# Kernel optimization log

Measured on AMD Instinct MI355X. Metric: run time of the kernel, lower is better.

## Reference

```python
import jax, jax.numpy as jnp
import numpy as np

N = 131072   # octree nodes at this depth
K = 27       # 3x3x3 kernel taps
CIN = 32
COUT = 32
EPS = 1e-5   # BatchNorm1d default eps


def setup_inputs() -> dict:
    key = jax.random.key(0)
    k1, k2, k3, k4, k5 = jax.random.split(key, 5)
    data = jax.random.normal(k1, (N, CIN), dtype=jnp.float32)
    # deconv weight: one [Cin, Cout] matrix per kernel tap
    weight = jax.random.normal(k2, (K, CIN, COUT), dtype=jnp.float32) * 0.05
    gamma = 1.0 + 0.1 * jax.random.normal(k3, (COUT,), dtype=jnp.float32)
    beta = 0.1 * jax.random.normal(k4, (COUT,), dtype=jnp.float32)
    # octree neighbor table: for each input node, the K output nodes it scatters into
    neigh = jax.random.randint(k5, (N, K), 0, N, dtype=jnp.int32)
    return {"data": data, "weight": weight, "gamma": gamma, "beta": beta, "neigh": neigh}


def reference(data, weight, gamma, beta, neigh):
    # Sparse transposed conv (stride=1): each node i produces a contribution
    # data[i] @ weight[k] that is scatter-added into output node neigh[i, k].
    contrib = jnp.einsum('ni,kio->nko', data, weight)          # [N, K, Cout]
    out = jax.ops.segment_sum(contrib.reshape(-1, COUT),
                              neigh.reshape(-1),
                              num_segments=N)                   # [N, Cout]
    # BatchNorm1d (training mode: batch statistics over the node dimension)
    mean = jnp.mean(out, axis=0)
    var = jnp.var(out, axis=0)
    y = gamma * (out - mean) * jax.lax.rsqrt(var + EPS) + beta
    # ReLU
    return jnp.maximum(y, 0.0)
```

## Files before the change

kernel.cpp:

```cpp
#include <hip/hip_runtime.h>
#include <hip/hip_bf16.h>
#include <hip/hip_fp16.h>

#define NN 131072
#define KK 27
#define CC 32
#define EPSV 1e-5f

#define WS_STATS 0
#define WS_ACC   256
#define WS_NEEDED ((size_t)WS_ACC + (size_t)NN * CC * 2)

typedef __bf16 bf16x8 __attribute__((ext_vector_type(8)));
typedef short s16x8 __attribute__((ext_vector_type(8)));
typedef float f32x4 __attribute__((ext_vector_type(4)));

__device__ inline unsigned short f2bf(float f) {
    unsigned int u = __float_as_uint(f);
    u += 0x7FFF + ((u >> 16) & 1);
    return (unsigned short)(u >> 16);
}

__global__ __launch_bounds__(256) void scatter_kernel(
    const float* __restrict__ data, const float* __restrict__ weight,
    const int* __restrict__ neigh, __half2* __restrict__ acc2)
{
    __shared__ unsigned short wfrag[KK * 2 * 64 * 8];

    const int tid = threadIdx.x;
    const int lane = tid & 63;
    const int wv = tid >> 6;
    const int node_base = blockIdx.x * 128;

    for (int p = tid; p < KK * 1024; p += 256) {
        const int k  = p >> 10;
        const int ci = (p >> 5) & 31;
        const int c  = p & 31;
        const unsigned short v = f2bf(weight[p]);
        const int chalf = c & 1;
        const int col   = c >> 1;
        const int fl = col | ((ci >> 3) << 4);
        const int j = ci & 7;
        wfrag[(((k << 1) | chalf) * 64 + fl) * 8 + j] = v;
    }

    const int quad = lane >> 4;
    const int m = lane & 15;
    s16x8 afr[2];
    #pragma unroll
    for (int g = 0; g < 2; ++g) {
        const int node = node_base + wv * 32 + g * 16 + m;
        const float* src = data + node * 32 + quad * 8;
        const float4 v0 = *(const float4*)(src);
        const float4 v1 = *(const float4*)(src + 4);
        s16x8 s;
        s[0] = (short)f2bf(v0.x); s[1] = (short)f2bf(v0.y);
        s[2] = (short)f2bf(v0.z); s[3] = (short)f2bf(v0.w);
        s[4] = (short)f2bf(v1.x); s[5] = (short)f2bf(v1.y);
        s[6] = (short)f2bf(v1.z); s[7] = (short)f2bf(v1.w);
        afr[g] = s;
    }

    __syncthreads();

    const int rq = quad << 2;
    const f32x4 zero = {0.f, 0.f, 0.f, 0.f};

    for (int k = 0; k < KK; ++k) {
        int nj[2][4];
        #pragma unroll
        for (int g = 0; g < 2; ++g)
            #pragma unroll
            for (int r = 0; r < 4; ++r) {
                const int node = node_base + wv * 32 + g * 16 + rq + r;
                nj[g][r] = neigh[node * KK + k];
            }
        const s16x8 bs0 = *(const s16x8*)&wfrag[(((k << 1) | 0) * 64 + lane) * 8];
        const s16x8 bs1 = *(const s16x8*)&wfrag[(((k << 1) | 1) * 64 + lane) * 8];
        #pragma unroll
        for (int g = 0; g < 2; ++g) {
            const f32x4 d0 = __builtin_amdgcn_mfma_f32_16x16x32_bf16(
                __builtin_bit_cast(bf16x8, afr[g]), __builtin_bit_cast(bf16x8, bs0),
                zero, 0, 0, 0);
            const f32x4 d1 = __builtin_amdgcn_mfma_f32_16x16x32_bf16(
                __builtin_bit_cast(bf16x8, afr[g]), __builtin_bit_cast(bf16x8, bs1),
                zero, 0, 0, 0);
            #pragma unroll
            for (int r = 0; r < 4; ++r) {
                __half2 v;
                v.x = __float2half(d0[r]);
                v.y = __float2half(d1[r]);
                unsafeAtomicAdd(&acc2[nj[g][r] * 16 + m], v);
            }
        }
    }
}

__global__ __launch_bounds__(256) void stats_kernel(
    const __half2* __restrict__ acc2, float* __restrict__ stats)
{
    __shared__ float ls[16][33], ls2[16][33];
    const int tid = threadIdx.x;
    const int c2 = tid & 15, rg = tid >> 4;
    float sx = 0.f, sy = 0.f, s2x = 0.f, s2y = 0.f;
    const int row0 = blockIdx.x * 512;
    for (int it = 0; it < 32; ++it) {
        const __half2 h = acc2[(row0 + it * 16 + rg) * 16 + c2];
        const float vx = __half2float(h.x), vy = __half2float(h.y);
        sx += vx; sy += vy; s2x += vx * vx; s2y += vy * vy;
    }
    ls[rg][2 * c2] = sx;  ls[rg][2 * c2 + 1] = sy;
    ls2[rg][2 * c2] = s2x; ls2[rg][2 * c2 + 1] = s2y;
    __syncthreads();
    if (tid < 32) {
        float S = 0.f, S2 = 0.f;
        #pragma unroll
        for (int g = 0; g < 16; ++g) { S += ls[g][tid]; S2 += ls2[g][tid]; }
        atomicAdd(&stats[tid], S);
        atomicAdd(&stats[32 + tid], S2);
    }
}

__global__ __launch_bounds__(256) void bn_relu_kernel(
    const __half2* __restrict__ acc2, float* __restrict__ out,
    const float* __restrict__ stats,
    const float* __restrict__ gamma, const float* __restrict__ beta)
{
    __shared__ float sc[32], sh[32];
    const int tid = threadIdx.x;
    if (tid < 32) {
        const float mean = stats[tid] * (1.0f / NN);
        const float var  = stats[32 + tid] * (1.0f / NN) - mean * mean;
        const float s = gamma[tid] * rsqrtf(var + EPSV);
        sc[tid] = s;
        sh[tid] = beta[tid] - mean * s;
    }
    __syncthreads();
    const int idx = blockIdx.x * 256 + tid;
    const int c0 = (idx & 3) << 3;
    const __half2 h4[4] = { acc2[idx * 4], acc2[idx * 4 + 1],
                            acc2[idx * 4 + 2], acc2[idx * 4 + 3] };
    float4 o0, o1;
    o0.x = fmaxf(__half2float(h4[0].x) * sc[c0]     + sh[c0],     0.f);
    o0.y = fmaxf(__half2float(h4[0].y) * sc[c0 + 1] + sh[c0 + 1], 0.f);
    o0.z = fmaxf(__half2float(h4[1].x) * sc[c0 + 2] + sh[c0 + 2], 0.f);
    o0.w = fmaxf(__half2float(h4[1].y) * sc[c0 + 3] + sh[c0 + 3], 0.f);
    o1.x = fmaxf(__half2float(h4[2].x) * sc[c0 + 4] + sh[c0 + 4], 0.f);
    o1.y = fmaxf(__half2float(h4[2].y) * sc[c0 + 5] + sh[c0 + 5], 0.f);
    o1.z = fmaxf(__half2float(h4[3].x) * sc[c0 + 6] + sh[c0 + 6], 0.f);
    o1.w = fmaxf(__half2float(h4[3].y) * sc[c0 + 7] + sh[c0 + 7], 0.f);
    ((float4*)out)[idx * 2]     = o0;
    ((float4*)out)[idx * 2 + 1] = o1;
}

__global__ __launch_bounds__(256) void scatter_f32_kernel(
    const float* __restrict__ data, const float* __restrict__ weight,
    const int* __restrict__ neigh, float* __restrict__ out)
{
    __shared__ unsigned short wfrag[KK * 2 * 64 * 8];
    const int tid = threadIdx.x;
    const int lane = tid & 63;
    const int wv = tid >> 6;
    const int node_base = blockIdx.x * 128;
    for (int p = tid; p < KK * 1024; p += 256) {
        const int k  = p >> 10;
        const int ci = (p >> 5) & 31;
        const int c  = p & 31;
        const unsigned short v = f2bf(weight[p]);
        const int chalf = c >> 4;
        const int fl = (c & 15) | ((ci >> 3) << 4);
        const int j = ci & 7;
        wfrag[(((k << 1) | chalf) * 64 + fl) * 8 + j] = v;
    }
    const int quad = lane >> 4;
    const int m = lane & 15;
    s16x8 afr[2];
    #pragma unroll
    for (int g = 0; g < 2; ++g) {
        const int node = node_base + wv * 32 + g * 16 + m;
        const float* src = data + node * 32 + quad * 8;
        const float4 v0 = *(const float4*)(src);
        const float4 v1 = *(const float4*)(src + 4);
        s16x8 s;
        s[0] = (short)f2bf(v0.x); s[1] = (short)f2bf(v0.y);
        s[2] = (short)f2bf(v0.z); s[3] = (short)f2bf(v0.w);
        s[4] = (short)f2bf(v1.x); s[5] = (short)f2bf(v1.y);
        s[6] = (short)f2bf(v1.z); s[7] = (short)f2bf(v1.w);
        afr[g] = s;
    }
    __syncthreads();
    const int rq = quad << 2;
    const f32x4 zero = {0.f, 0.f, 0.f, 0.f};
    for (int k = 0; k < KK; ++k) {
        int nj[2][4];
        #pragma unroll
        for (int g = 0; g < 2; ++g)
            #pragma unroll
            for (int r = 0; r < 4; ++r) {
                const int node = node_base + wv * 32 + g * 16 + rq + r;
                nj[g][r] = neigh[node * KK + k];
            }
        #pragma unroll
        for (int ch = 0; ch < 2; ++ch) {
            const s16x8 bs = *(const s16x8*)&wfrag[((((k << 1) | ch)) * 64 + lane) * 8];
            const bf16x8 bfr = __builtin_bit_cast(bf16x8, bs);
            const int c = (ch << 4) | m;
            #pragma unroll
            for (int g = 0; g < 2; ++g) {
                f32x4 a2 = __builtin_amdgcn_mfma_f32_16x16x32_bf16(
                    __builtin_bit_cast(bf16x8, afr[g]), bfr, zero, 0, 0, 0);
                #pragma unroll
                for (int r = 0; r < 4; ++r)
                    __hip_atomic_fetch_add(&out[nj[g][r] * 32 + c], a2[r],
                                           __ATOMIC_RELAXED, __HIP_MEMORY_SCOPE_AGENT);
            }
        }
    }
}

__global__ __launch_bounds__(256) void stats_f32_kernel(
    const float* __restrict__ out, float* __restrict__ stats)
{
    __shared__ float ls[256], ls2[256];
    const int tid = threadIdx.x;
    const int c = tid & 31, rg = tid >> 5;
    float s = 0.f, s2 = 0.f;
    const int row0 = blockIdx.x * 512;
    for (int it = 0; it < 64; ++it) {
        const float v = out[(row0 + it * 8 + rg) * 32 + c];
        s += v; s2 += v * v;
    }
    ls[tid] = s; ls2[tid] = s2;
    __syncthreads();
    if (tid < 32) {
        float S = 0.f, S2 = 0.f;
        #pragma unroll
        for (int r = 0; r < 8; ++r) { S += ls[r * 32 + tid]; S2 += ls2[r * 32 + tid]; }
        atomicAdd(&stats[tid], S);
        atomicAdd(&stats[32 + tid], S2);
    }
}

__global__ __launch_bounds__(256) void bn_relu_f32_kernel(
    float* __restrict__ out, const float* __restrict__ stats,
    const float* __restrict__ gamma, const float* __restrict__ beta)
{
    __shared__ float sc[32], sh[32];
    const int tid = threadIdx.x;
    if (tid < 32) {
        const float mean = stats[tid] * (1.0f / NN);
        const float var  = stats[32 + tid] * (1.0f / NN) - mean * mean;
        const float s = gamma[tid] * rsqrtf(var + EPSV);
        sc[tid] = s;
        sh[tid] = beta[tid] - mean * s;
    }
    __syncthreads();
    const int idx = blockIdx.x * 256 + tid;
    float4 v = ((float4*)out)[idx];
    const int cb = (idx & 7) << 2;
    v.x = fmaxf(v.x * sc[cb]     + sh[cb],     0.f);
    v.y = fmaxf(v.y * sc[cb + 1] + sh[cb + 1], 0.f);
    v.z = fmaxf(v.z * sc[cb + 2] + sh[cb + 2], 0.f);
    v.w = fmaxf(v.w * sc[cb + 3] + sh[cb + 3], 0.f);
    ((float4*)out)[idx] = v;
}

extern "C" void kernel_launch(void* const* d_in, const int* in_sizes, int n_in,
                              void* d_out, int out_size, void* d_ws, size_t ws_size,
                              hipStream_t stream) {
    const float* data   = (const float*)d_in[0];
    const float* weight = (const float*)d_in[1];
    const float* gamma  = (const float*)d_in[2];
    const float* beta   = (const float*)d_in[3];
    const int*   neigh  = (const int*)d_in[4];
    float* out = (float*)d_out;
    char* ws = (char*)d_ws;
    float* stats = (float*)(ws + WS_STATS);

    if (ws_size >= WS_NEEDED) {
        __half2* acc2 = (__half2*)(ws + WS_ACC);
        hipMemsetAsync(ws, 0, WS_NEEDED, stream);
        scatter_kernel<<<NN / 128, 256, 0, stream>>>(data, weight, neigh, acc2);
        stats_kernel<<<NN / 512, 256, 0, stream>>>(acc2, stats);
        bn_relu_kernel<<<(NN * CC / 8) / 256, 256, 0, stream>>>(acc2, out, stats, gamma, beta);
    } else {
        hipMemsetAsync(out, 0, (size_t)NN * CC * sizeof(float), stream);
        hipMemsetAsync(stats, 0, 64 * sizeof(float), stream);
        scatter_f32_kernel<<<NN / 128, 256, 0, stream>>>(data, weight, neigh, out);
        stats_f32_kernel<<<NN / 512, 256, 0, stream>>>(out, stats);
        bn_relu_f32_kernel<<<(NN * CC / 4) / 256, 256, 0, stream>>>(out, stats, gamma, beta);
    }
}
```

Measured before the change: 271.6 us.

## Precompute bf16 weight fragments once and software-pipeline neighbor/weight loads

Adds a small prep kernel that converts and permutes the weights into MFMA fragment layout in workspace once, so each of the 1024 scatter blocks no longer rebuilds a 55KB LDS copy and waits on a barrier. The scatter kernel now reads weight fragments straight from global/L2 and prefetches the next tap's neighbor indices and weight fragments while the current tap's MFMAs and atomics run. This removes the per-block prologue and frees LDS for occupancy, at the cost of an extra launch, two memsets instead of one, and L2 traffic for the weight reads.

```diff
diff --git a/kernel.cpp b/kernel.cpp
--- a/kernel.cpp
+++ b/kernel.cpp
@@ -8,7 +8,8 @@
 #define EPSV 1e-5f
 
 #define WS_STATS 0
-#define WS_ACC   256
+#define WS_WPERM 256
+#define WS_ACC   65536
 #define WS_NEEDED ((size_t)WS_ACC + (size_t)NN * CC * 2)
 
 typedef __bf16 bf16x8 __attribute__((ext_vector_type(8)));
@@ -21,29 +22,186 @@
     return (unsigned short)(u >> 16);
 }
 
+__global__ __launch_bounds__(256) void prep_weights_kernel(
+    const float* __restrict__ weight, unsigned short* __restrict__ wperm)
+{
+    const int p = blockIdx.x * 256 + threadIdx.x;
+    if (p >= KK * 1024) return;
+    const int k  = p >> 10;
+    const int ci = (p >> 5) & 31;
+    const int c  = p & 31;
+    const unsigned short v = f2bf(weight[p]);
+    const int chalf = c & 1;
+    const int col   = c >> 1;
+    const int fl = col | ((ci >> 3) << 4);
+    const int j = ci & 7;
+    wperm[(((k << 1) | chalf) * 64 + fl) * 8 + j] = v;
+}
+
 __global__ __launch_bounds__(256) void scatter_kernel(
+    const float* __restrict__ data, const unsigned short* __restrict__ wperm,
+    const int* __restrict__ neigh, __half2* __restrict__ acc2)
+{
+    const int tid = threadIdx.x;
+    const int lane = tid & 63;
+    const int wv = tid >> 6;
+    const int node_base = blockIdx.x * 128 + wv * 32;
+
+    const int quad = lane >> 4;
+    const int m = lane & 15;
+    const int rq = quad << 2;
+
+    s16x8 afr[2];
+    #pragma unroll
+    for (int g = 0; g < 2; ++g) {
+        const int node = node_base + g * 16 + m;
+        const float* src = data + node * 32 + quad * 8;
+        const float4 v0 = *(const float4*)(src);
+        const float4 v1 = *(const float4*)(src + 4);
+        s16x8 s;
+        s[0] = (short)f2bf(v0.x); s[1] = (short)f2bf(v0.y);
+        s[2] = (short)f2bf(v0.z); s[3] = (short)f2bf(v0.w);
+        s[4] = (short)f2bf(v1.x); s[5] = (short)f2bf(v1.y);
+        s[6] = (short)f2bf(v1.z); s[7] = (short)f2bf(v1.w);
+        afr[g] = s;
+    }
+
+    const s16x8* wp = (const s16x8*)wperm;
+    const f32x4 zero = {0.f, 0.f, 0.f, 0.f};
+
+    int nj0[4], nj1[4];
+    #pragma unroll
+    for (int r = 0; r < 4; ++r) {
+        nj0[r] = neigh[(node_base + rq + r) * KK];
+        nj1[r] = neigh[(node_base + 16 + rq + r) * KK];
+    }
+    s16x8 bs0 = wp[lane];
+    s16x8 bs1 = wp[64 + lane];
+
+    for (int k = 0; k < KK; ++k) {
+        const int kn = (k < KK - 1) ? k + 1 : k;
+        int nn0[4], nn1[4];
+        #pragma unroll
+        for (int r = 0; r < 4; ++r) {
+            nn0[r] = neigh[(node_base + rq + r) * KK + kn];
+            nn1[r] = neigh[(node_base + 16 + rq + r) * KK + kn];
+        }
+        const s16x8 nbs0 = wp[(kn * 2) * 64 + lane];
+        const s16x8 nbs1 = wp[(kn * 2 + 1) * 64 + lane];
+
+        {
+            const f32x4 d0 = __builtin_amdgcn_mfma_f32_16x16x32_bf16(
+                __builtin_bit_cast(bf16x8, afr[0]), __builtin_bit_cast(bf16x8, bs0),
+                zero, 0, 0, 0);
+            const f32x4 d1 = __builtin_amdgcn_mfma_f32_16x16x32_bf16(
+                __builtin_bit_cast(bf16x8, afr[0]), __builtin_bit_cast(bf16x8, bs1),
+                zero, 0, 0, 0);
+            #pragma unroll
+            for (int r = 0; r < 4; ++r) {
+                __half2 v;
+                v.x = __float2half(d0[r]);
+                v.y = __float2half(d1[r]);
+                unsafeAtomicAdd(&acc2[nj0[r] * 16 + m], v);
+            }
+        }
+        {
+            const f32x4 d0 = __builtin_amdgcn_mfma_f32_16x16x32_bf16(
+                __builtin_bit_cast(bf16x8, afr[1]), __builtin_bit_cast(bf16x8, bs0),
+                zero, 0, 0, 0);
+            const f32x4 d1 = __builtin_amdgcn_mfma_f32_16x16x32_bf16(
+                __builtin_bit_cast(bf16x8, afr[1]), __builtin_bit_cast(bf16x8, bs1),
+                zero, 0, 0, 0);
+            #pragma unroll
+            for (int r = 0; r < 4; ++r) {
+                __half2 v;
+                v.x = __float2half(d0[r]);
+                v.y = __float2half(d1[r]);
+                unsafeAtomicAdd(&acc2[nj1[r] * 16 + m], v);
+            }
+        }
+
+        bs0 = nbs0; bs1 = nbs1;
+        #pragma unroll
+        for (int r = 0; r < 4; ++r) { nj0[r] = nn0[r]; nj1[r] = nn1[r]; }
+    }
+}
+
+__global__ __launch_bounds__(256) void stats_kernel(
+    const __half2* __restrict__ acc2, float* __restrict__ stats)
+{
+    __shared__ float ls[16][33], ls2[16][33];
+    const int tid = threadIdx.x;
+    const int c2 = tid & 15, rg = tid >> 4;
+    float sx = 0.f, sy = 0.f, s2x = 0.f, s2y = 0.f;
+    const int row0 = blockIdx.x * 512;
+    for (int it = 0; it < 32; ++it) {
+        const __half2 h = acc2[(row0 + it * 16 + rg) * 16 + c2];
+        const float vx = __half2float(h.x), vy = __half2float(h.y);
+        sx += vx; sy += vy; s2x += vx * vx; s2y += vy * vy;
+    }
+    ls[rg][2 * c2] = sx;  ls[rg][2 * c2 + 1] = sy;
+    ls2[rg][2 * c2] = s2x; ls2[rg][2 * c2 + 1] = s2y;
+    __syncthreads();
+    if (tid < 32) {
+        float S = 0.f, S2 = 0.f;
+        #pragma unroll
+        for (int g = 0; g < 16; ++g) { S += ls[g][tid]; S2 += ls2[g][tid]; }
+        atomicAdd(&stats[tid], S);
+        atomicAdd(&stats[32 + tid], S2);
+    }
+}
+
+__global__ __launch_bounds__(256) void bn_relu_kernel(
+    const __half2* __restrict__ acc2, float* __restrict__ out,
+    const float* __restrict__ stats,
+    const float* __restrict__ gamma, const float* __restrict__ beta)
+{
+    __shared__ float sc[32], sh[32];
+    const int tid = threadIdx.x;
+    if (tid < 32) {
+        const float mean = stats[tid] * (1.0f / NN);
+        const float var  = stats[32 + tid] * (1.0f / NN) - mean * mean;
+        const float s = gamma[tid] * rsqrtf(var + EPSV);
+        sc[tid] = s;
+        sh[tid] = beta[tid] - mean * s;
+    }
+    __syncthreads();
+    const int idx = blockIdx.x * 256 + tid;
+    const int c0 = (idx & 3) << 3;
+    const __half2 h4[4] = { acc2[idx * 4], acc2[idx * 4 + 1],
+                            acc2[idx * 4 + 2], acc2[idx * 4 + 3] };
+    float4 o0, o1;
+    o0.x = fmaxf(__half2float(h4[0].x) * sc[c0]     + sh[c0],     0.f);
+    o0.y = fmaxf(__half2float(h4[0].y) * sc[c0 + 1] + sh[c0 + 1], 0.f);
+    o0.z = fmaxf(__half2float(h4[1].x) * sc[c0 + 2] + sh[c0 + 2], 0.f);
+    o0.w = fmaxf(__half2float(h4[1].y) * sc[c0 + 3] + sh[c0 + 3], 0.f);
+    o1.x = fmaxf(__half2float(h4[2].x) * sc[c0 + 4] + sh[c0 + 4], 0.f);
+    o1.y = fmaxf(__half2float(h4[2].y) * sc[c0 + 5] + sh[c0 + 5], 0.f);
+    o1.z = fmaxf(__half2float(h4[3].x) * sc[c0 + 6] + sh[c0 + 6], 0.f);
+    o1.w = fmaxf(__half2float(h4[3].y) * sc[c0 + 7] + sh[c0 + 7], 0.f);
+    ((float4*)out)[idx * 2]     = o0;
+    ((float4*)out)[idx * 2 + 1] = o1;
+}
+
+__global__ __launch_bounds__(256) void scatter_f32_kernel(
     const float* __restrict__ data, const float* __restrict__ weight,
-    const int* __restrict__ neigh, __half2* __restrict__ acc2)
+    const int* __restrict__ neigh, float* __restrict__ out)
 {
     __shared__ unsigned short wfrag[KK * 2 * 64 * 8];
-
     const int tid = threadIdx.x;
     const int lane = tid & 63;
     const int wv = tid >> 6;
     const int node_base = blockIdx.x * 128;
-
     for (int p = tid; p < KK * 1024; p += 256) {
         const int k  = p >> 10;
         const int ci = (p >> 5) & 31;
         const int c  = p & 31;
         const unsigned short v = f2bf(weight[p]);
-        const int chalf = c & 1;
-        const int col   = c >> 1;
-        const int fl = col | ((ci >> 3) << 4);
+        const int chalf = c >> 4;
+        const int fl = (c & 15) | ((ci >> 3) << 4);
         const int j = ci & 7;
         wfrag[(((k << 1) | chalf) * 64 + fl) * 8 + j] = v;
     }
-
     const int quad = lane >> 4;
     const int m = lane & 15;
     s16x8 afr[2];
@@ -60,134 +218,6 @@
         s[6] = (short)f2bf(v1.z); s[7] = (short)f2bf(v1.w);
         afr[g] = s;
     }
-
-    __syncthreads();
-
-    const int rq = quad << 2;
-    const f32x4 zero = {0.f, 0.f, 0.f, 0.f};
-
-    for (int k = 0; k < KK; ++k) {
-        int nj[2][4];
-        #pragma unroll
-        for (int g = 0; g < 2; ++g)
-            #pragma unroll
-            for (int r = 0; r < 4; ++r) {
-                const int node = node_base + wv * 32 + g * 16 + rq + r;
-                nj[g][r] = neigh[node * KK + k];
-            }
-        const s16x8 bs0 = *(const s16x8*)&wfrag[(((k << 1) | 0) * 64 + lane) * 8];
-        const s16x8 bs1 = *(const s16x8*)&wfrag[(((k << 1) | 1) * 64 + lane) * 8];
-        #pragma unroll
-        for (int g = 0; g < 2; ++g) {
-            const f32x4 d0 = __builtin_amdgcn_mfma_f32_16x16x32_bf16(
-                __builtin_bit_cast(bf16x8, afr[g]), __builtin_bit_cast(bf16x8, bs0),
-                zero, 0, 0, 0);
-            const f32x4 d1 = __builtin_amdgcn_mfma_f32_16x16x32_bf16(
-                __builtin_bit_cast(bf16x8, afr[g]), __builtin_bit_cast(bf16x8, bs1),
-                zero, 0, 0, 0);
-            #pragma unroll
-            for (int r = 0; r < 4; ++r) {
-                __half2 v;
-                v.x = __float2half(d0[r]);
-                v.y = __float2half(d1[r]);
-                unsafeAtomicAdd(&acc2[nj[g][r] * 16 + m], v);
-            }
-        }
-    }
-}
-
-__global__ __launch_bounds__(256) void stats_kernel(
-    const __half2* __restrict__ acc2, float* __restrict__ stats)
-{
-    __shared__ float ls[16][33], ls2[16][33];
-    const int tid = threadIdx.x;
-    const int c2 = tid & 15, rg = tid >> 4;
-    float sx = 0.f, sy = 0.f, s2x = 0.f, s2y = 0.f;
-    const int row0 = blockIdx.x * 512;
-    for (int it = 0; it < 32; ++it) {
-        const __half2 h = acc2[(row0 + it * 16 + rg) * 16 + c2];
-        const float vx = __half2float(h.x), vy = __half2float(h.y);
-        sx += vx; sy += vy; s2x += vx * vx; s2y += vy * vy;
-    }
-    ls[rg][2 * c2] = sx;  ls[rg][2 * c2 + 1] = sy;
-    ls2[rg][2 * c2] = s2x; ls2[rg][2 * c2 + 1] = s2y;
-    __syncthreads();
-    if (tid < 32) {
-        float S = 0.f, S2 = 0.f;
-        #pragma unroll
-        for (int g = 0; g < 16; ++g) { S += ls[g][tid]; S2 += ls2[g][tid]; }
-        atomicAdd(&stats[tid], S);
-        atomicAdd(&stats[32 + tid], S2);
-    }
-}
-
-__global__ __launch_bounds__(256) void bn_relu_kernel(
-    const __half2* __restrict__ acc2, float* __restrict__ out,
-    const float* __restrict__ stats,
-    const float* __restrict__ gamma, const float* __restrict__ beta)
-{
-    __shared__ float sc[32], sh[32];
-    const int tid = threadIdx.x;
-    if (tid < 32) {
-        const float mean = stats[tid] * (1.0f / NN);
-        const float var  = stats[32 + tid] * (1.0f / NN) - mean * mean;
-        const float s = gamma[tid] * rsqrtf(var + EPSV);
-        sc[tid] = s;
-        sh[tid] = beta[tid] - mean * s;
-    }
-    __syncthreads();
-    const int idx = blockIdx.x * 256 + tid;
-    const int c0 = (idx & 3) << 3;
-    const __half2 h4[4] = { acc2[idx * 4], acc2[idx * 4 + 1],
-                            acc2[idx * 4 + 2], acc2[idx * 4 + 3] };
-    float4 o0, o1;
-    o0.x = fmaxf(__half2float(h4[0].x) * sc[c0]     + sh[c0],     0.f);
-    o0.y = fmaxf(__half2float(h4[0].y) * sc[c0 + 1] + sh[c0 + 1], 0.f);
-    o0.z = fmaxf(__half2float(h4[1].x) * sc[c0 + 2] + sh[c0 + 2], 0.f);
-    o0.w = fmaxf(__half2float(h4[1].y) * sc[c0 + 3] + sh[c0 + 3], 0.f);
-    o1.x = fmaxf(__half2float(h4[2].x) * sc[c0 + 4] + sh[c0 + 4], 0.f);
-    o1.y = fmaxf(__half2float(h4[2].y) * sc[c0 + 5] + sh[c0 + 5], 0.f);
-    o1.z = fmaxf(__half2float(h4[3].x) * sc[c0 + 6] + sh[c0 + 6], 0.f);
-    o1.w = fmaxf(__half2float(h4[3].y) * sc[c0 + 7] + sh[c0 + 7], 0.f);
-    ((float4*)out)[idx * 2]     = o0;
-    ((float4*)out)[idx * 2 + 1] = o1;
-}
-
-__global__ __launch_bounds__(256) void scatter_f32_kernel(
-    const float* __restrict__ data, const float* __restrict__ weight,
-    const int* __restrict__ neigh, float* __restrict__ out)
-{
-    __shared__ unsigned short wfrag[KK * 2 * 64 * 8];
-    const int tid = threadIdx.x;
-    const int lane = tid & 63;
-    const int wv = tid >> 6;
-    const int node_base = blockIdx.x * 128;
-    for (int p = tid; p < KK * 1024; p += 256) {
-        const int k  = p >> 10;
-        const int ci = (p >> 5) & 31;
-        const int c  = p & 31;
-        const unsigned short v = f2bf(weight[p]);
-        const int chalf = c >> 4;
-        const int fl = (c & 15) | ((ci >> 3) << 4);
-        const int j = ci & 7;
-        wfrag[(((k << 1) | chalf) * 64 + fl) * 8 + j] = v;
-    }
-    const int quad = lane >> 4;
-    const int m = lane & 15;
-    s16x8 afr[2];
-    #pragma unroll
-    for (int g = 0; g < 2; ++g) {
-        const int node = node_base + wv * 32 + g * 16 + m;
-        const float* src = data + node * 32 + quad * 8;
-        const float4 v0 = *(const float4*)(src);
-        const float4 v1 = *(const float4*)(src + 4);
-        s16x8 s;
-        s[0] = (short)f2bf(v0.x); s[1] = (short)f2bf(v0.y);
-        s[2] = (short)f2bf(v0.z); s[3] = (short)f2bf(v0.w);
-        s[4] = (short)f2bf(v1.x); s[5] = (short)f2bf(v1.y);
-        s[6] = (short)f2bf(v1.z); s[7] = (short)f2bf(v1.w);
-        afr[g] = s;
-    }
     __syncthreads();
     const int rq = quad << 2;
     const f32x4 zero = {0.f, 0.f, 0.f, 0.f};
@@ -279,8 +309,11 @@
 
     if (ws_size >= WS_NEEDED) {
         __half2* acc2 = (__half2*)(ws + WS_ACC);
-        hipMemsetAsync(ws, 0, WS_NEEDED, stream);
-        scatter_kernel<<<NN / 128, 256, 0, stream>>>(data, weight, neigh, acc2);
+        unsigned short* wperm = (unsigned short*)(ws + WS_WPERM);
+        hipMemsetAsync(ws + WS_STATS, 0, 256, stream);
+        hipMemsetAsync(ws + WS_ACC, 0, (size_t)NN * CC * 2, stream);
+        prep_weights_kernel<<<(KK * 1024 + 255) / 256, 256, 0, stream>>>(weight, wperm);
+        scatter_kernel<<<NN / 128, 256, 0, stream>>>(data, wperm, neigh, acc2);
         stats_kernel<<<NN / 512, 256, 0, stream>>>(acc2, stats);
         bn_relu_kernel<<<(NN * CC / 8) / 256, 256, 0, stream>>>(acc2, out, stats, gamma, beta);
     } else {
```

Measured after the change: 271.4 us. Within noise of the previous version (-0.1%).
